# Kernel optimization log

Hardware: AMD Instinct MI355X
Metric: run time of the kernel (lower is better)

The kernel has to match this reference:

```python
import jax, jax.numpy as jnp
import numpy as np

B = 16384
R, N_NODES, K, N_LAYERS, LATENT = 5, 68, 32, 3, 68


def setup_inputs() -> dict:
    key = jax.random.key(0)
    ks = jax.random.split(key, 6)
    z = jax.random.normal(ks[0], (B, LATENT), dtype=jnp.float32)
    adjacency = jax.random.randint(ks[1], (N_NODES, K), 0, N_NODES)
    # init_fc weights stored as [latent, n_nodes] so forward is z @ fc_w[r] + fc_b[r]
    fc_w = jax.random.normal(ks[2], (R, LATENT, N_NODES), dtype=jnp.float32) * 0.1
    fc_b = jax.random.normal(ks[3], (R, N_NODES), dtype=jnp.float32) * 0.1
    gcn_w = jax.random.normal(ks[4], (R, N_LAYERS, N_NODES, K), dtype=jnp.float32) * 0.1
    gcn_b = jax.random.normal(ks[5], (R, N_LAYERS, N_NODES), dtype=jnp.float32) * 0.1
    return {"z": z, "adjacency": adjacency, "fc_w": fc_w, "fc_b": fc_b,
            "gcn_w": gcn_w, "gcn_b": gcn_b}


def _gcn_layer(x, adjacency, w, b):
    # x: [B, N]; adjacency: [N, K] int; w: [N, K]; b: [N]
    x_nb = x[:, adjacency]                      # [B, N, K] ragged-style gather
    val = jnp.einsum('bnk,nk->bn', x_nb, w) + b  # per-node weighted neighbor sum
    return jax.nn.sigmoid(val)


def reference(z, adjacency, fc_w, fc_b, gcn_w, gcn_b):
    b = z.shape[0]
    sc_sum = jnp.zeros((b, N_NODES, N_NODES), dtype=z.dtype)
    for r in range(R):
        x = z @ fc_w[r] + fc_b[r]               # init_fc[r]
        for l in range(N_LAYERS):
            x = _gcn_layer(x, adjacency, gcn_w[r, l], gcn_b[r, l])
        # rank-1 outer product per sample: bmm(x.unsqueeze(2), x.unsqueeze(1))
        sc_sum = sc_sum + x[:, :, None] * x[:, None, :]
    sc_sum = 0.5 * (sc_sum + jnp.swapaxes(sc_sum, 1, 2))
    return sc_sum.reshape(b, -1)
```

## Files before the change

kernel.cpp:

```cpp
#include <hip/hip_runtime.h>
#include <math.h>

#define R_ 5
#define NN 68
#define KK 32
#define NL 3
#define LAT 68
#define NSL 17
#define ROWQ (NN / 4)
#define NF4 ((NN * NN) / 4)
#define BBK2 16
#define LSTR 344
#define NPREP (R_ * NL)

__global__ __launch_bounds__(256) void prep_k(
    const float* __restrict__ z, const int* __restrict__ adj,
    const float* __restrict__ gw, float* __restrict__ wd,
    float* __restrict__ zT, int B) {
  const int t = threadIdx.x;
  if (blockIdx.x < NPREP) {
    const int rl = blockIdx.x;
    __shared__ float col[NN][NN + 4];
    for (int i = t; i < NN * (NN + 4); i += 256) (&col[0][0])[i] = 0.0f;
    __syncthreads();
    if (t < NN) {
      const int n = t;
      const int* ar = adj + n * KK;
      const float* wr = gw + ((size_t)rl * NN + n) * KK;
      for (int k = 0; k < KK; ++k) col[ar[k]][n] += wr[k];
    }
    __syncthreads();
    float* wout = wd + (size_t)rl * NN * NN;
    for (int i = t; i < NN * NN; i += 256) {
      const int m = i / NN, n = i - m * NN;
      wout[i] = col[m][n];
    }
  } else {
    const int b0 = (blockIdx.x - NPREP) * 64;
    __shared__ float zls[64][LAT + 1];
    for (int idx = t; idx < 64 * ROWQ; idx += 256) {
      const int row = idx / ROWQ, q = idx - row * ROWQ;
      const float4 v =
          *reinterpret_cast<const float4*>(z + (size_t)(b0 + row) * LAT + 4 * q);
      zls[row][4 * q + 0] = v.x;
      zls[row][4 * q + 1] = v.y;
      zls[row][4 * q + 2] = v.z;
      zls[row][4 * q + 3] = v.w;
    }
    __syncthreads();
    for (int idx = t; idx < LAT * 64; idx += 256) {
      const int l = idx >> 6, bb = idx & 63;
      zT[(size_t)l * B + b0 + bb] = zls[bb][l];
    }
  }
}

__global__ __launch_bounds__(256) void chain_k(
    const float* __restrict__ zT, const float* __restrict__ fc_w,
    const float* __restrict__ fc_b, const float* __restrict__ wd,
    const float* __restrict__ gb, float* __restrict__ X, int B, int nb) {
  const int t = threadIdx.x;
  const int lane = t & 63;
  const int w = __builtin_amdgcn_readfirstlane(t >> 6);
  const int n0 = w * NSL;
  const int r = blockIdx.x / nb;
  const int b0 = (blockIdx.x - r * nb) * 64;

  __shared__ float xs[NN][64];

  for (int idx = t; idx < NN * 64; idx += 256) {
    const int m = idx >> 6;
    xs[m][idx & 63] = zT[(size_t)m * B + b0 + (idx & 63)];
  }
  __syncthreads();

  float acc[NSL];

#pragma unroll 1
  for (int stage = 0; stage < 1 + NL; ++stage) {
    const float* wb = (stage == 0) ? fc_w + (size_t)r * LAT * NN
                                   : wd + (size_t)(r * NL + stage - 1) * NN * NN;
    const float* bias = (stage == 0) ? fc_b + r * NN
                                     : gb + (size_t)(r * NL + stage - 1) * NN;
#pragma unroll
    for (int j = 0; j < NSL; ++j) acc[j] = bias[n0 + j];

#pragma unroll 1
    for (int mb = 0; mb < 4; ++mb) {
      float xmv[NSL];
#pragma unroll
      for (int k = 0; k < NSL; ++k) xmv[k] = xs[mb * NSL + k][lane];
      const float* wrb = wb + (size_t)(mb * NSL) * NN + n0;
#pragma unroll
      for (int k = 0; k < NSL; ++k) {
        const float* wr = wrb + (size_t)k * NN;
#pragma unroll
        for (int j = 0; j < NSL; ++j) acc[j] = fmaf(xmv[k], wr[j], acc[j]);
      }
    }
    if (stage > 0) {
#pragma unroll
      for (int j = 0; j < NSL; ++j)
        acc[j] = 1.0f / (1.0f + __expf(-acc[j]));
    }
    if (stage < NL) {
      __syncthreads();
#pragma unroll
      for (int j = 0; j < NSL; ++j) xs[n0 + j][lane] = acc[j];
      __syncthreads();
    }
  }

  float* Xb = X + ((size_t)r * NN + n0) * B + b0 + lane;
#pragma unroll
  for (int j = 0; j < NSL; ++j) Xb[(size_t)j * B] = acc[j];
}

__global__ __launch_bounds__(256) void outer_k(const float* __restrict__ X,
                                               float* __restrict__ out, int B) {
  const int t = threadIdx.x;
  const int b0 = blockIdx.x * BBK2;
  __shared__ float xls[BBK2 * LSTR];

  for (int idx = t; idx < R_ * NN * BBK2; idx += 256) {
    const int rn = idx >> 4, bb = idx & (BBK2 - 1);
    xls[bb * LSTR + rn] = X[(size_t)rn * B + b0 + bb];
  }
  __syncthreads();

  float4* ob = reinterpret_cast<float4*>(out) + (size_t)b0 * NF4;
  const int total = BBK2 * NF4;
#pragma unroll 1
  for (int base = t; base < total; base += 1024) {
    float4 av[4];
#pragma unroll
    for (int u = 0; u < 4; ++u) {
      const int fg = base + u * 256;
      if (fg < total) {
        const int bb = fg / NF4;
        const int f = fg - bb * NF4;
        const int i = f / ROWQ;
        const int q = f - i * ROWQ;
        const float* xb = &xls[bb * LSTR];
        float4 a = make_float4(0.f, 0.f, 0.f, 0.f);
#pragma unroll
        for (int r = 0; r < R_; ++r) {
          const float xi = xb[r * NN + i];
          const float4 xj =
              *reinterpret_cast<const float4*>(xb + r * NN + 4 * q);
          a.x = fmaf(xi, xj.x, a.x);
          a.y = fmaf(xi, xj.y, a.y);
          a.z = fmaf(xi, xj.z, a.z);
          a.w = fmaf(xi, xj.w, a.w);
        }
        av[u] = a;
      }
    }
#pragma unroll
    for (int u = 0; u < 4; ++u) {
      const int fg = base + u * 256;
      if (fg < total) ob[fg] = av[u];
    }
  }
}

extern "C" void kernel_launch(void* const* d_in, const int* in_sizes, int n_in,
                              void* d_out, int out_size, void* d_ws, size_t ws_size,
                              hipStream_t stream) {
  const float* z    = (const float*)d_in[0];
  const int*   adj  = (const int*)  d_in[1];
  const float* fc_w = (const float*)d_in[2];
  const float* fc_b = (const float*)d_in[3];
  const float* gw   = (const float*)d_in[4];
  const float* gb   = (const float*)d_in[5];
  float* out = (float*)d_out;

  const int B = in_sizes[0] / LAT;
  float* wd = (float*)d_ws;
  float* zT = wd + R_ * NL * NN * NN;
  float* X  = zT + (size_t)LAT * B;

  const int nb = B / 64;

  prep_k<<<NPREP + B / 64, 256, 0, stream>>>(z, adj, gw, wd, zT, B);
  chain_k<<<R_ * nb, 256, 0, stream>>>(zT, fc_w, fc_b, wd, gb, X, B, nb);
  outer_k<<<B / BBK2, 256, 0, stream>>>(X, out, B);
}
```

Before: 124.4 us.

## Pad chain weights to 80 columns and read them as float4 per-lane vectors

The prep kernel now writes all four stage weight matrices and biases into one padded [68x80] workspace layout. The chain kernel splits the output columns across waves as 20 columns each and loads weights as 16-byte vector loads, replacing the 17-wide scalar slices. A vzero VGPR offset forces those loads to per-lane vector memory rather than scalar loads. This aims to cut load instruction count and improve weight fetch efficiency in the dense chain stage. The cost is some wasted FMAs on padded columns (80 vs 68) and the last wave idling on 12 of its 20 columns.

```diff
diff --git a/kernel.cpp b/kernel.cpp
--- a/kernel.cpp
+++ b/kernel.cpp
@@ -6,20 +6,26 @@
 #define KK 32
 #define NL 3
 #define LAT 68
-#define NSL 17
+#define NPAD 80
 #define ROWQ (NN / 4)
 #define NF4 ((NN * NN) / 4)
 #define BBK2 16
 #define LSTR 344
 #define NPREP (R_ * NL)
+#define WPAD_FLOATS (R_ * 4 * NN * NPAD)
+#define BPAD_FLOATS (R_ * 4 * NPAD)
 
 __global__ __launch_bounds__(256) void prep_k(
     const float* __restrict__ z, const int* __restrict__ adj,
-    const float* __restrict__ gw, float* __restrict__ wd,
+    const float* __restrict__ fc_w, const float* __restrict__ fc_b,
+    const float* __restrict__ gw, const float* __restrict__ gb,
+    float* __restrict__ wpad, float* __restrict__ bpad,
     float* __restrict__ zT, int B) {
   const int t = threadIdx.x;
   if (blockIdx.x < NPREP) {
     const int rl = blockIdx.x;
+    const int r = rl / NL, l = rl - r * NL;
+    const int stage = 1 + l;
     __shared__ float col[NN][NN + 4];
     for (int i = t; i < NN * (NN + 4); i += 256) (&col[0][0])[i] = 0.0f;
     __syncthreads();
@@ -30,13 +36,28 @@
       for (int k = 0; k < KK; ++k) col[ar[k]][n] += wr[k];
     }
     __syncthreads();
-    float* wout = wd + (size_t)rl * NN * NN;
-    for (int i = t; i < NN * NN; i += 256) {
-      const int m = i / NN, n = i - m * NN;
-      wout[i] = col[m][n];
+    float* wout = wpad + (size_t)((r * 4 + stage) * NN) * NPAD;
+    for (int i = t; i < NN * NPAD; i += 256) {
+      const int m = i / NPAD, n = i - m * NPAD;
+      wout[i] = (n < NN) ? col[m][n] : 0.0f;
+    }
+  } else if (blockIdx.x < NPREP + R_) {
+    const int r = blockIdx.x - NPREP;
+    float* wout = wpad + (size_t)((r * 4 + 0) * NN) * NPAD;
+    for (int i = t; i < NN * NPAD; i += 256) {
+      const int m = i / NPAD, n = i - m * NPAD;
+      wout[i] = (n < NN) ? fc_w[((size_t)r * NN + m) * NN + n] : 0.0f;
+    }
+    for (int i = t; i < 4 * NPAD; i += 256) {
+      const int st = i / NPAD, n = i - st * NPAD;
+      float v = 0.0f;
+      if (n < NN)
+        v = (st == 0) ? fc_b[r * NN + n]
+                      : gb[((size_t)r * NL + st - 1) * NN + n];
+      bpad[(r * 4 + st) * NPAD + n] = v;
     }
   } else {
-    const int b0 = (blockIdx.x - NPREP) * 64;
+    const int b0 = (blockIdx.x - (NPREP + R_)) * 64;
     __shared__ float zls[64][LAT + 1];
     for (int idx = t; idx < 64 * ROWQ; idx += 256) {
       const int row = idx / ROWQ, q = idx - row * ROWQ;
@@ -56,13 +77,12 @@
 }
 
 __global__ __launch_bounds__(256) void chain_k(
-    const float* __restrict__ zT, const float* __restrict__ fc_w,
-    const float* __restrict__ fc_b, const float* __restrict__ wd,
-    const float* __restrict__ gb, float* __restrict__ X, int B, int nb) {
+    const float* __restrict__ zT, const float* __restrict__ wpad,
+    const float* __restrict__ bpad, float* __restrict__ X, int B, int nb) {
   const int t = threadIdx.x;
   const int lane = t & 63;
   const int w = __builtin_amdgcn_readfirstlane(t >> 6);
-  const int n0 = w * NSL;
+  const int c0 = 20 * w;
   const int r = blockIdx.x / nb;
   const int b0 = (blockIdx.x - r * nb) * 64;
 
@@ -74,46 +94,77 @@
   }
   __syncthreads();
 
-  float acc[NSL];
+  int vzero;
+  asm("v_mov_b32 %0, 0" : "=v"(vzero));
+
+  float4 acc[5];
 
 #pragma unroll 1
   for (int stage = 0; stage < 1 + NL; ++stage) {
-    const float* wb = (stage == 0) ? fc_w + (size_t)r * LAT * NN
-                                   : wd + (size_t)(r * NL + stage - 1) * NN * NN;
-    const float* bias = (stage == 0) ? fc_b + r * NN
-                                     : gb + (size_t)(r * NL + stage - 1) * NN;
-#pragma unroll
-    for (int j = 0; j < NSL; ++j) acc[j] = bias[n0 + j];
-
-#pragma unroll 1
-    for (int mb = 0; mb < 4; ++mb) {
-      float xmv[NSL];
-#pragma unroll
-      for (int k = 0; k < NSL; ++k) xmv[k] = xs[mb * NSL + k][lane];
-      const float* wrb = wb + (size_t)(mb * NSL) * NN + n0;
-#pragma unroll
-      for (int k = 0; k < NSL; ++k) {
-        const float* wr = wrb + (size_t)k * NN;
-#pragma unroll
-        for (int j = 0; j < NSL; ++j) acc[j] = fmaf(xmv[k], wr[j], acc[j]);
+    const float* wbS =
+        wpad + (size_t)((r * 4 + stage) * NN) * NPAD + c0 + vzero;
+    const float* bpS = bpad + (r * 4 + stage) * NPAD + c0 + vzero;
+#pragma unroll
+    for (int j = 0; j < 5; ++j)
+      acc[j] = *reinterpret_cast<const float4*>(bpS + 4 * j);
+
+#pragma unroll 4
+    for (int m = 0; m < NN; ++m) {
+      const float xm = xs[m][lane];
+      const float* wr = wbS + m * NPAD;
+#pragma unroll
+      for (int j = 0; j < 5; ++j) {
+        const float4 ww = *reinterpret_cast<const float4*>(wr + 4 * j);
+        acc[j].x = fmaf(xm, ww.x, acc[j].x);
+        acc[j].y = fmaf(xm, ww.y, acc[j].y);
+        acc[j].z = fmaf(xm, ww.z, acc[j].z);
+        acc[j].w = fmaf(xm, ww.w, acc[j].w);
       }
     }
     if (stage > 0) {
 #pragma unroll
-      for (int j = 0; j < NSL; ++j)
-        acc[j] = 1.0f / (1.0f + __expf(-acc[j]));
+      for (int j = 0; j < 5; ++j) {
+        acc[j].x = 1.0f / (1.0f + __expf(-acc[j].x));
+        acc[j].y = 1.0f / (1.0f + __expf(-acc[j].y));
+        acc[j].z = 1.0f / (1.0f + __expf(-acc[j].z));
+        acc[j].w = 1.0f / (1.0f + __expf(-acc[j].w));
+      }
     }
     if (stage < NL) {
       __syncthreads();
-#pragma unroll
-      for (int j = 0; j < NSL; ++j) xs[n0 + j][lane] = acc[j];
+      if (w < 3) {
+#pragma unroll
+        for (int j = 0; j < 5; ++j) {
+          const int n0c = c0 + 4 * j;
+          xs[n0c + 0][lane] = acc[j].x;
+          xs[n0c + 1][lane] = acc[j].y;
+          xs[n0c + 2][lane] = acc[j].z;
+          xs[n0c + 3][lane] = acc[j].w;
+        }
+      } else {
+#pragma unroll
+        for (int j = 0; j < 2; ++j) {
+          const int n0c = 60 + 4 * j;
+          xs[n0c + 0][lane] = acc[j].x;
+          xs[n0c + 1][lane] = acc[j].y;
+          xs[n0c + 2][lane] = acc[j].z;
+          xs[n0c + 3][lane] = acc[j].w;
+        }
+      }
       __syncthreads();
     }
   }
 
-  float* Xb = X + ((size_t)r * NN + n0) * B + b0 + lane;
-#pragma unroll
-  for (int j = 0; j < NSL; ++j) Xb[(size_t)j * B] = acc[j];
+  float* Xb = X + ((size_t)r * NN + c0) * B + b0 + lane;
+  if (w < 3) {
+#pragma unroll
+    for (int j = 0; j < 20; ++j)
+      Xb[(size_t)j * B] = reinterpret_cast<const float*>(&acc[j >> 2])[j & 3];
+  } else {
+#pragma unroll
+    for (int j = 0; j < 8; ++j)
+      Xb[(size_t)j * B] = reinterpret_cast<const float*>(&acc[j >> 2])[j & 3];
+  }
 }
 
 __global__ __launch_bounds__(256) void outer_k(const float* __restrict__ X,
@@ -176,13 +227,15 @@
   float* out = (float*)d_out;
 
   const int B = in_sizes[0] / LAT;
-  float* wd = (float*)d_ws;
-  float* zT = wd + R_ * NL * NN * NN;
+  float* wpad = (float*)d_ws;
+  float* bpad = wpad + WPAD_FLOATS;
+  float* zT = bpad + BPAD_FLOATS;
   float* X  = zT + (size_t)LAT * B;
 
   const int nb = B / 64;
 
-  prep_k<<<NPREP + B / 64, 256, 0, stream>>>(z, adj, gw, wd, zT, B);
-  chain_k<<<R_ * nb, 256, 0, stream>>>(zT, fc_w, fc_b, wd, gb, X, B, nb);
+  prep_k<<<NPREP + R_ + B / 64, 256, 0, stream>>>(z, adj, fc_w, fc_b, gw, gb,
+                                                  wpad, bpad, zT, B);
+  chain_k<<<R_ * nb, 256, 0, stream>>>(zT, wpad, bpad, X, B, nb);
   outer_k<<<B / BBK2, 256, 0, stream>>>(X, out, B);
 }
```

New measurement: 282.8 us. 127% more time.
